# Optimization experiments

Measured on AMD Instinct MI355X. Metric: run time of the kernel, lower is better.

Reference implementation:

```python
import jax, jax.numpy as jnp
import numpy as np

N, E = 10000, 160000
F_IN, H1, C1, C2 = 256, 8, 128, 128
SLOPE = 0.2  # PyG GATConv default negative_slope


def setup_inputs() -> dict:
    key = jax.random.key(0)
    ks = jax.random.split(key, 9)
    s = 0.05
    return {
        "x": jax.random.normal(ks[0], (N, F_IN), jnp.float32),
        "edge_index": jax.random.randint(ks[1], (2, E), 0, N),
        "W1": jax.random.normal(ks[2], (F_IN, H1 * C1), jnp.float32) * s,
        "a_src1": jax.random.normal(ks[3], (H1, C1), jnp.float32) * s,
        "a_dst1": jax.random.normal(ks[4], (H1, C1), jnp.float32) * s,
        "b1": jnp.zeros((H1 * C1,), jnp.float32),
        "W2": jax.random.normal(ks[5], (H1 * C1, C2), jnp.float32) * s,
        "a_src2": jax.random.normal(ks[6], (1, C2), jnp.float32) * s,
        "a_dst2": jax.random.normal(ks[7], (1, C2), jnp.float32) * s,
        "b2": jnp.zeros((C2,), jnp.float32),
    }


def gat_conv(x, src, dst, W, a_s, a_d, b, heads, out_ch, concat):
    n = x.shape[0]
    h = (x @ W).reshape(n, heads, out_ch)            # [N,H,C]
    s_src = jnp.einsum("nhc,hc->nh", h, a_s)         # [N,H]
    s_dst = jnp.einsum("nhc,hc->nh", h, a_d)
    e = jax.nn.leaky_relu(s_src[src] + s_dst[dst], SLOPE)   # [Etot,H]
    # segment softmax over incoming edges per destination (self-loops guarantee non-empty segments)
    m = jax.lax.stop_gradient(jax.ops.segment_max(e, dst, num_segments=n))
    p = jnp.exp(e - m[dst])
    denom = jax.ops.segment_sum(p, dst, num_segments=n)
    alpha = p / denom[dst]                            # [Etot,H]
    out = jax.ops.segment_sum(h[src] * alpha[:, :, None], dst, num_segments=n)  # [N,H,C]
    out = out.reshape(n, heads * out_ch) if concat else out.mean(axis=1)
    return out + b


def reference(x, edge_index, W1, a_src1, a_dst1, b1, W2, a_src2, a_dst2, b2):
    n = x.shape[0]
    loops = jnp.arange(n, dtype=edge_index.dtype)     # PyG add_self_loops=True
    src = jnp.concatenate([edge_index[0], loops])
    dst = jnp.concatenate([edge_index[1], loops])
    # dropout layers are identity at inference (training=False)
    h1 = jax.nn.elu(gat_conv(x, src, dst, W1, a_src1, a_dst1, b1, H1, C1, True))
    return gat_conv(h1, src, dst, W2, a_src2, a_dst2, b2, 1, C2, False)
```

## Files before the change

### kernel.cpp

```cpp
#include <hip/hip_runtime.h>
#include <math.h>

#define F_IN 256
#define H1 8
#define C1 128
#define HC1 1024
#define C2 128
#define SLOPE 0.2f

typedef unsigned short u16;
typedef __attribute__((ext_vector_type(8))) short bf16x8;
typedef __attribute__((ext_vector_type(4))) float f32x4;
typedef __attribute__((ext_vector_type(2))) float f32x2;


__device__ __forceinline__ float lrelu(float v) { return v > 0.f ? v : SLOPE * v; }

__device__ __forceinline__ unsigned bf16_rne(float x) {
    unsigned u = __float_as_uint(x);
    u += 0x7fffu + ((u >> 16) & 1u);
    return u >> 16;
}

__device__ __forceinline__ void split2(float a, float b, unsigned& hi, unsigned& lo) {
    unsigned ha = bf16_rne(a), hb = bf16_rne(b);
    float fa = __uint_as_float(ha << 16), fb = __uint_as_float(hb << 16);
    hi = ha | (hb << 16);
    lo = bf16_rne(a - fa) | (bf16_rne(b - fb) << 16);
}

__device__ __forceinline__ void gload16(const u16* g, u16* l) {
    __builtin_amdgcn_global_load_lds(
        (const __attribute__((address_space(1))) unsigned*)g,
        (__attribute__((address_space(3))) unsigned*)l, 16, 0, 0);
}


__global__ void init_deg(int* deg, int n) {
    int i = blockIdx.x * blockDim.x + threadIdx.x;
    if (i < n) deg[i] = 1;
}

__global__ void hist_kernel(const int* __restrict__ dst, int* __restrict__ deg, int E) {
    int i = blockIdx.x * blockDim.x + threadIdx.x;
    if (i < E) atomicAdd(&deg[dst[i]], 1);
}

__global__ void scan_kernel(const int* __restrict__ deg, int* __restrict__ start,
                            int* __restrict__ cursor, int n) {
    __shared__ int buf[1024];
    int carry = 0;
    for (int base = 0; base < n; base += 1024) {
        int i = base + (int)threadIdx.x;
        int v = (i < n) ? deg[i] : 0;
        buf[threadIdx.x] = v;
        __syncthreads();
        for (int offd = 1; offd < 1024; offd <<= 1) {
            int tv = 0;
            if ((int)threadIdx.x >= offd) tv = buf[threadIdx.x - offd];
            __syncthreads();
            if ((int)threadIdx.x >= offd) buf[threadIdx.x] += tv;
            __syncthreads();
        }
        int incl = buf[threadIdx.x];
        if (i < n) { start[i] = carry + incl - v; cursor[i] = carry + incl - v; }
        carry += buf[1023];
        __syncthreads();
    }
    if (threadIdx.x == 0) start[n] = carry;
}

__global__ void scatter_kernel(const int* __restrict__ src, const int* __restrict__ dst,
                               int* __restrict__ cursor, int* __restrict__ ssorted,
                               int E, int N) {
    int i = blockIdx.x * blockDim.x + threadIdx.x;
    if (i < E) {
        int d = dst[i];
        int pos = atomicAdd(&cursor[d], 1);
        ssorted[pos] = src[i];
    } else if (i < E + N) {
        int d = i - E;
        int pos = atomicAdd(&cursor[d], 1);
        ssorted[pos] = d;
    }
}


__global__ void split_mat(const float* __restrict__ in, u16* __restrict__ hi,
                          u16* __restrict__ lo, int n) {
    int i = blockIdx.x * blockDim.x + threadIdx.x;
    if (i >= n) return;
    float v = in[i];
    unsigned h = bf16_rne(v);
    hi[i] = (u16)h;
    lo[i] = (u16)bf16_rne(v - __uint_as_float(h << 16));
}

__global__ void split_transpose(const float* __restrict__ in, u16* __restrict__ hi,
                                u16* __restrict__ lo, int R, int C) {
    int i = blockIdx.x * blockDim.x + threadIdx.x;
    if (i >= R * C) return;
    int r = i / C, c = i % C;
    float v = in[i];
    unsigned h = bf16_rne(v);
    hi[(size_t)c * R + r] = (u16)h;
    lo[(size_t)c * R + r] = (u16)bf16_rne(v - __uint_as_float(h << 16));
}


__global__ __launch_bounds__(256) void gemm_mfma(const u16* __restrict__ Ahi,
                                                 const u16* __restrict__ Alo,
                                                 const u16* __restrict__ Bhi,
                                                 const u16* __restrict__ Blo,
                                                 u16* __restrict__ Cbf,
                                                 int M, int N, int K) {
    __shared__ u16 lds[16384];
    const int t = threadIdx.x;
    const int rbase = blockIdx.y * 128;
    const int cbase = blockIdx.x * 128;

    const int lane = t & 63;
    const int R0 = (t >> 7) << 6;
    const int C0 = ((t >> 6) & 1) << 6;
    const int lrow = lane & 15;
    const int kq = lane >> 4;

    f32x4 acc[4][4] = {};

    for (int k0 = 0; k0 < K; k0 += 32) {
#pragma unroll
        for (int i = 0; i < 2; i++) {
            int c = t + (i << 8);
            int row = c >> 2;
            int kc = (c & 3) << 3;
            int ar = min(rbase + row, M - 1);
            int br = cbase + row;
            gload16(Ahi + (size_t)ar * K + k0 + kc, &lds[c * 8]);
            gload16(Alo + (size_t)ar * K + k0 + kc, &lds[4096 + c * 8]);
            gload16(Bhi + (size_t)br * K + k0 + kc, &lds[8192 + c * 8]);
            gload16(Blo + (size_t)br * K + k0 + kc, &lds[12288 + c * 8]);
        }
        __syncthreads();

        bf16x8 ah[4], al[4], bh[4], bl[4];
#pragma unroll
        for (int m = 0; m < 4; m++) {
            int off = (R0 + (m << 4) + lrow) * 32 + (kq << 3);
            ah[m] = *(const bf16x8*)&lds[off];
            al[m] = *(const bf16x8*)&lds[4096 + off];
        }
#pragma unroll
        for (int n = 0; n < 4; n++) {
            int off = (C0 + (n << 4) + lrow) * 32 + (kq << 3);
            bh[n] = *(const bf16x8*)&lds[8192 + off];
            bl[n] = *(const bf16x8*)&lds[12288 + off];
        }
#pragma unroll
        for (int m = 0; m < 4; m++)
#pragma unroll
            for (int n = 0; n < 4; n++) {
                acc[m][n] = __builtin_amdgcn_mfma_f32_16x16x32_bf16(ah[m], bh[n], acc[m][n], 0, 0, 0);
                acc[m][n] = __builtin_amdgcn_mfma_f32_16x16x32_bf16(ah[m], bl[n], acc[m][n], 0, 0, 0);
                acc[m][n] = __builtin_amdgcn_mfma_f32_16x16x32_bf16(al[m], bh[n], acc[m][n], 0, 0, 0);
            }
        __syncthreads();
    }

#pragma unroll
    for (int m = 0; m < 4; m++)
#pragma unroll
        for (int n = 0; n < 4; n++) {
            int col = cbase + C0 + (n << 4) + lrow;
#pragma unroll
            for (int r = 0; r < 4; r++) {
                int row = rbase + R0 + (m << 4) + kq * 4 + r;
                if (row < M) Cbf[(size_t)row * N + col] = (u16)bf16_rne(acc[m][n][r]);
            }
        }
}


__global__ __launch_bounds__(256) void gemm_mfma64(const u16* __restrict__ Ahi,
                                                   const u16* __restrict__ Alo,
                                                   const u16* __restrict__ Bhi,
                                                   const u16* __restrict__ Blo,
                                                   u16* __restrict__ Cbf,
                                                   int M, int N, int K) {
    __shared__ u16 lds[8192];
    const int t = threadIdx.x;
    const int rbase = blockIdx.y * 64;
    const int cbase = blockIdx.x * 64;

    const int lane = t & 63;
    const int w = t >> 6;
    const int R0 = (w >> 1) << 5;
    const int C0 = (w & 1) << 5;
    const int lrow = lane & 15;
    const int kq = lane >> 4;

    f32x4 acc[2][2] = {};

    for (int k0 = 0; k0 < K; k0 += 32) {
        {
            int row = t >> 2;
            int kc = (t & 3) << 3;
            int ar = min(rbase + row, M - 1);
            int br = cbase + row;
            gload16(Ahi + (size_t)ar * K + k0 + kc, &lds[t * 8]);
            gload16(Alo + (size_t)ar * K + k0 + kc, &lds[2048 + t * 8]);
            gload16(Bhi + (size_t)br * K + k0 + kc, &lds[4096 + t * 8]);
            gload16(Blo + (size_t)br * K + k0 + kc, &lds[6144 + t * 8]);
        }
        __syncthreads();

        bf16x8 ah[2], al[2], bh[2], bl[2];
#pragma unroll
        for (int m = 0; m < 2; m++) {
            int off = (R0 + (m << 4) + lrow) * 32 + (kq << 3);
            ah[m] = *(const bf16x8*)&lds[off];
            al[m] = *(const bf16x8*)&lds[2048 + off];
        }
#pragma unroll
        for (int n = 0; n < 2; n++) {
            int off = (C0 + (n << 4) + lrow) * 32 + (kq << 3);
            bh[n] = *(const bf16x8*)&lds[4096 + off];
            bl[n] = *(const bf16x8*)&lds[6144 + off];
        }
#pragma unroll
        for (int m = 0; m < 2; m++)
#pragma unroll
            for (int n = 0; n < 2; n++) {
                acc[m][n] = __builtin_amdgcn_mfma_f32_16x16x32_bf16(ah[m], bh[n], acc[m][n], 0, 0, 0);
                acc[m][n] = __builtin_amdgcn_mfma_f32_16x16x32_bf16(ah[m], bl[n], acc[m][n], 0, 0, 0);
                acc[m][n] = __builtin_amdgcn_mfma_f32_16x16x32_bf16(al[m], bh[n], acc[m][n], 0, 0, 0);
            }
        __syncthreads();
    }

#pragma unroll
    for (int m = 0; m < 2; m++)
#pragma unroll
        for (int n = 0; n < 2; n++) {
            int col = cbase + C0 + (n << 4) + lrow;
#pragma unroll
            for (int r = 0; r < 4; r++) {
                int row = rbase + R0 + (m << 4) + kq * 4 + r;
                if (row < M) Cbf[(size_t)row * N + col] = (u16)bf16_rne(acc[m][n][r]);
            }
        }
}


__global__ __launch_bounds__(256) void scores1_bf(const unsigned* __restrict__ hbf,
                                                  const float* __restrict__ a_s,
                                                  const float* __restrict__ a_d,
                                                  float* __restrict__ ssrc,
                                                  float* __restrict__ sdst, int N) {
    int wid = blockIdx.x * 4 + (threadIdx.x >> 6);
    if (wid >= N * H1) return;
    int lane = threadIdx.x & 63;
    int n = wid >> 3, hh = wid & 7;
    unsigned u = hbf[(size_t)n * 512 + hh * 64 + lane];
    float c0 = __uint_as_float(u << 16);
    float c1 = __uint_as_float(u & 0xffff0000u);
    const float* as = a_s + hh * C1;
    const float* ad = a_d + hh * C1;
    float vs = c0 * as[2 * lane] + c1 * as[2 * lane + 1];
    float vd = c0 * ad[2 * lane] + c1 * ad[2 * lane + 1];
    for (int off = 32; off; off >>= 1) {
        vs += __shfl_xor(vs, off);
        vd += __shfl_xor(vd, off);
    }
    if (lane == 0) { ssrc[wid] = vs; sdst[wid] = vd; }
}

__global__ __launch_bounds__(256) void scores2_bf(const unsigned* __restrict__ hbf,
                                                  const float* __restrict__ a_s,
                                                  const float* __restrict__ a_d,
                                                  float* __restrict__ ssrc,
                                                  float* __restrict__ sdst, int N) {
    int n = blockIdx.x * 4 + (threadIdx.x >> 6);
    if (n >= N) return;
    int lane = threadIdx.x & 63;
    unsigned u = hbf[(size_t)n * 64 + lane];
    float c0 = __uint_as_float(u << 16);
    float c1 = __uint_as_float(u & 0xffff0000u);
    float vs = c0 * a_s[2 * lane] + c1 * a_s[2 * lane + 1];
    float vd = c0 * a_d[2 * lane] + c1 * a_d[2 * lane + 1];
    for (int off = 32; off; off >>= 1) {
        vs += __shfl_xor(vs, off);
        vd += __shfl_xor(vd, off);
    }
    if (lane == 0) { ssrc[n] = vs; sdst[n] = vd; }
}


template<int H, bool SPLITOUT>
__global__ __launch_bounds__(256) void agg_bf(const unsigned* __restrict__ hbf,
                                              const float* __restrict__ ssrc,
                                              const float* __restrict__ sdst,
                                              const int* __restrict__ start,
                                              const int* __restrict__ ssorted,
                                              const float* __restrict__ bias,
                                              float* __restrict__ out,
                                              unsigned* __restrict__ outHi,
                                              unsigned* __restrict__ outLo, int N) {
    constexpr int CH = 128;
    __shared__ int2 pairs[4][CH + 4];
    int hh, grp;
    if (H == 8) { hh = blockIdx.x & 7; grp = blockIdx.x >> 3; }
    else        { hh = 0;              grp = blockIdx.x; }
    int wid = threadIdx.x >> 6, lane = threadIdx.x & 63;
    int d = grp * 4 + wid;
    if (d >= N) return;
    const int g = lane >> 4, p = lane & 15;
    int s0 = start[d];
    int ne = start[d + 1] - s0;
    float sd = sdst[d * H + hh];
    const int rowbytes = H * 256;
    const char* hbase = (const char*)hbf + hh * 256 + p * 16;

    float m = -1e30f;
    for (int e = lane; e < ne; e += 64)
        m = fmaxf(m, lrelu(ssrc[ssorted[s0 + e] * H + hh] + sd));
    for (int o = 32; o; o >>= 1) m = fmaxf(m, __shfl_xor(m, o));

    float ssum = 0.f;
    for (int e = lane; e < ne; e += 64)
        ssum += __expf(lrelu(ssrc[ssorted[s0 + e] * H + hh] + sd) - m);
    for (int o = 32; o; o >>= 1) ssum += __shfl_xor(ssum, o);
    float inv = 1.f / ssum;

    f32x2 acc0 = {0.f, 0.f}, acc1 = {0.f, 0.f}, acc2 = {0.f, 0.f}, acc3 = {0.f, 0.f};
    for (int c0 = 0; c0 < ne; c0 += CH) {
        int cn = min(CH, ne - c0);
        int cn4 = (cn + 3) & ~3;
        for (int e = lane; e < cn4; e += 64) {
            int2 pr = make_int2(0, 0);
            if (e < cn) {
                int sr = ssorted[s0 + c0 + e];
                float a = __expf(lrelu(ssrc[sr * H + hh] + sd) - m) * inv;
                pr = make_int2(sr * rowbytes, __float_as_int(a));
            }
            pairs[wid][e] = pr;
        }
#pragma unroll 2
        for (int e2 = 0; e2 < cn4; e2 += 4) {
            int2 pr = pairs[wid][e2 + g];
            float a = __int_as_float(pr.y);
            uint4 u = *(const uint4*)(hbase + pr.x);
            f32x2 av = {a, a};
            f32x2 f0 = {__uint_as_float(u.x << 16), __uint_as_float(u.x & 0xffff0000u)};
            f32x2 f1 = {__uint_as_float(u.y << 16), __uint_as_float(u.y & 0xffff0000u)};
            f32x2 f2 = {__uint_as_float(u.z << 16), __uint_as_float(u.z & 0xffff0000u)};
            f32x2 f3 = {__uint_as_float(u.w << 16), __uint_as_float(u.w & 0xffff0000u)};
            acc0 += av * f0;
            acc1 += av * f1;
            acc2 += av * f2;
            acc3 += av * f3;
        }
    }

    float acc[8] = {acc0.x, acc0.y, acc1.x, acc1.y, acc2.x, acc2.y, acc3.x, acc3.y};
#pragma unroll
    for (int i = 0; i < 8; i++) {
        acc[i] += __shfl_xor(acc[i], 16);
        acc[i] += __shfl_xor(acc[i], 32);
    }

    float r0 = g == 0 ? acc[0] : g == 1 ? acc[2] : g == 2 ? acc[4] : acc[6];
    float r1 = g == 0 ? acc[1] : g == 1 ? acc[3] : g == 2 ? acc[5] : acc[7];
    int j = 4 * p + g;
    float2 bv = ((const float2*)bias)[hh * 64 + j];
    r0 += bv.x; r1 += bv.y;
    size_t idx = (size_t)d * (H * 64) + hh * 64 + j;
    if (SPLITOUT) {
        r0 = r0 > 0.f ? r0 : expm1f(r0);
        r1 = r1 > 0.f ? r1 : expm1f(r1);
        unsigned hi, lo;
        split2(r0, r1, hi, lo);
        outHi[idx] = hi;
        outLo[idx] = lo;
    } else {
        ((float2*)out)[idx] = make_float2(r0, r1);
    }
}


extern "C" void kernel_launch(void* const* d_in, const int* in_sizes, int n_in,
                              void* d_out, int out_size, void* d_ws, size_t ws_size,
                              hipStream_t stream) {
    const float* x      = (const float*)d_in[0];
    const int*   ei     = (const int*)d_in[1];
    const float* W1     = (const float*)d_in[2];
    const float* a_src1 = (const float*)d_in[3];
    const float* a_dst1 = (const float*)d_in[4];
    const float* b1     = (const float*)d_in[5];
    const float* W2     = (const float*)d_in[6];
    const float* a_src2 = (const float*)d_in[7];
    const float* a_dst2 = (const float*)d_in[8];
    const float* b2     = (const float*)d_in[9];
    float* out = (float*)d_out;

    int E = in_sizes[1] / 2;
    int N = in_sizes[0] / F_IN;
    const int* esrc = ei;
    const int* edst = ei + E;

    char* ws = (char*)d_ws;
    size_t off = 0;
    auto alloc = [&](size_t bytes) -> char* {
        char* p = ws + off;
        off = (off + bytes + 255) & ~(size_t)255;
        return p;
    };
    u16* x_hi    = (u16*)alloc((size_t)N * F_IN * 2);
    u16* x_lo    = (u16*)alloc((size_t)N * F_IN * 2);
    u16* W1t_hi  = (u16*)alloc((size_t)F_IN * HC1 * 2);
    u16* W1t_lo  = (u16*)alloc((size_t)F_IN * HC1 * 2);
    u16* W2t_hi  = (u16*)alloc((size_t)HC1 * C2 * 2);
    u16* W2t_lo  = (u16*)alloc((size_t)HC1 * C2 * 2);
    u16* h1_bf   = (u16*)alloc((size_t)N * HC1 * 2);
    u16* h1a_hi  = (u16*)alloc((size_t)N * HC1 * 2);
    u16* h1a_lo  = (u16*)alloc((size_t)N * HC1 * 2);
    u16* h2_bf   = (u16*)alloc((size_t)N * C2 * 2);
    float* ss1   = (float*)alloc((size_t)N * H1 * 4);
    float* sd1   = (float*)alloc((size_t)N * H1 * 4);
    float* ss2   = (float*)alloc((size_t)N * 4);
    float* sd2   = (float*)alloc((size_t)N * 4);
    int* deg     = (int*)alloc((size_t)N * 4);
    int* startp  = (int*)alloc((size_t)(N + 1) * 4);
    int* cursor  = (int*)alloc((size_t)N * 4);
    int* ssorted = (int*)alloc((size_t)(E + N) * 4);

    init_deg<<<(N + 255) / 256, 256, 0, stream>>>(deg, N);
    hist_kernel<<<(E + 255) / 256, 256, 0, stream>>>(edst, deg, E);
    scan_kernel<<<1, 1024, 0, stream>>>(deg, startp, cursor, N);
    scatter_kernel<<<(E + N + 255) / 256, 256, 0, stream>>>(esrc, edst, cursor, ssorted, E, N);

    split_mat<<<(N * F_IN + 255) / 256, 256, 0, stream>>>(x, x_hi, x_lo, N * F_IN);
    split_transpose<<<(F_IN * HC1 + 255) / 256, 256, 0, stream>>>(W1, W1t_hi, W1t_lo, F_IN, HC1);
    split_transpose<<<(HC1 * C2 + 255) / 256, 256, 0, stream>>>(W2, W2t_hi, W2t_lo, HC1, C2);

    gemm_mfma<<<dim3(HC1 / 128, (N + 127) / 128), 256, 0, stream>>>(
        x_hi, x_lo, W1t_hi, W1t_lo, h1_bf, N, HC1, F_IN);
    scores1_bf<<<(N * H1 + 3) / 4, 256, 0, stream>>>(
        (const unsigned*)h1_bf, a_src1, a_dst1, ss1, sd1, N);
    agg_bf<H1, true><<<((N + 3) / 4) * H1, 256, 0, stream>>>(
        (const unsigned*)h1_bf, ss1, sd1, startp, ssorted, b1,
        nullptr, (unsigned*)h1a_hi, (unsigned*)h1a_lo, N);

    gemm_mfma64<<<dim3(C2 / 64, (N + 63) / 64), 256, 0, stream>>>(
        h1a_hi, h1a_lo, W2t_hi, W2t_lo, h2_bf, N, C2, HC1);
    scores2_bf<<<(N + 3) / 4, 256, 0, stream>>>(
        (const unsigned*)h2_bf, a_src2, a_dst2, ss2, sd2, N);
    agg_bf<1, false><<<(N + 3) / 4, 256, 0, stream>>>(
        (const unsigned*)h2_bf, ss2, sd2, startp, ssorted, b2,
        out, nullptr, nullptr, N);
}
```

Measured before the change: 261.1 us.

## Precompute edge softmax numerators and denominators in separate kernels, drop max pass

Splits the per-destination aggregation into three stages. An edge-parallel kernel computes exp(leaky_relu(score)) for all heads, a per-node kernel sums these into inverse denominators, and a gather kernel reads the precomputed weights directly. The max-subtraction pass and the shared-memory pair staging are removed, which relies on the scores staying small enough that exp does not overflow. It adds extra launches, a dsorted array and an Et×8 float intermediate buffer with more global memory traffic.

```diff
diff --git a/kernel.cpp b/kernel.cpp
--- a/kernel.cpp
+++ b/kernel.cpp
@@ -72,16 +72,18 @@
 
 __global__ void scatter_kernel(const int* __restrict__ src, const int* __restrict__ dst,
                                int* __restrict__ cursor, int* __restrict__ ssorted,
-                               int E, int N) {
+                               int* __restrict__ dsorted, int E, int N) {
     int i = blockIdx.x * blockDim.x + threadIdx.x;
     if (i < E) {
         int d = dst[i];
         int pos = atomicAdd(&cursor[d], 1);
         ssorted[pos] = src[i];
+        dsorted[pos] = d;
     } else if (i < E + N) {
         int d = i - E;
         int pos = atomicAdd(&cursor[d], 1);
         ssorted[pos] = d;
+        dsorted[pos] = d;
     }
 }
 
@@ -295,70 +297,106 @@
 }
 
 
-template<int H, bool SPLITOUT>
-__global__ __launch_bounds__(256) void agg_bf(const unsigned* __restrict__ hbf,
+__global__ __launch_bounds__(256) void edgep1(const int* __restrict__ ssorted,
+                                              const int* __restrict__ dsorted,
                                               const float* __restrict__ ssrc,
                                               const float* __restrict__ sdst,
+                                              float* __restrict__ p, int Et) {
+    int e = blockIdx.x * 256 + threadIdx.x;
+    if (e >= Et) return;
+    int sr = ssorted[e], dr = dsorted[e];
+    float4 s0 = ((const float4*)(ssrc + sr * 8))[0];
+    float4 s1 = ((const float4*)(ssrc + sr * 8))[1];
+    float4 d0 = ((const float4*)(sdst + dr * 8))[0];
+    float4 d1 = ((const float4*)(sdst + dr * 8))[1];
+    float4 r0, r1;
+    r0.x = __expf(lrelu(s0.x + d0.x));
+    r0.y = __expf(lrelu(s0.y + d0.y));
+    r0.z = __expf(lrelu(s0.z + d0.z));
+    r0.w = __expf(lrelu(s0.w + d0.w));
+    r1.x = __expf(lrelu(s1.x + d1.x));
+    r1.y = __expf(lrelu(s1.y + d1.y));
+    r1.z = __expf(lrelu(s1.z + d1.z));
+    r1.w = __expf(lrelu(s1.w + d1.w));
+    ((float4*)(p + (size_t)e * 8))[0] = r0;
+    ((float4*)(p + (size_t)e * 8))[1] = r1;
+}
+
+__global__ __launch_bounds__(256) void edgep2(const int* __restrict__ ssorted,
+                                              const int* __restrict__ dsorted,
+                                              const float* __restrict__ ssrc,
+                                              const float* __restrict__ sdst,
+                                              float* __restrict__ p, int Et) {
+    int e = blockIdx.x * 256 + threadIdx.x;
+    if (e >= Et) return;
+    p[e] = __expf(lrelu(ssrc[ssorted[e]] + sdst[dsorted[e]]));
+}
+
+
+__global__ __launch_bounds__(256) void denom1(const float* __restrict__ p,
                                               const int* __restrict__ start,
-                                              const int* __restrict__ ssorted,
-                                              const float* __restrict__ bias,
-                                              float* __restrict__ out,
-                                              unsigned* __restrict__ outHi,
-                                              unsigned* __restrict__ outLo, int N) {
-    constexpr int CH = 128;
-    __shared__ int2 pairs[4][CH + 4];
+                                              float* __restrict__ dinv, int N) {
+    int t = blockIdx.x * 256 + threadIdx.x;
+    if (t >= N * 8) return;
+    int d = t >> 3, h = t & 7;
+    int s0 = start[d], ne = start[d + 1] - s0;
+    float s = 0.f;
+    for (int e = 0; e < ne; e++) s += p[(size_t)(s0 + e) * 8 + h];
+    dinv[t] = 1.f / s;
+}
+
+__global__ __launch_bounds__(256) void denom2(const float* __restrict__ p,
+                                              const int* __restrict__ start,
+                                              float* __restrict__ dinv, int N) {
+    int d = blockIdx.x * 256 + threadIdx.x;
+    if (d >= N) return;
+    int s0 = start[d], ne = start[d + 1] - s0;
+    float s = 0.f;
+    for (int e = 0; e < ne; e++) s += p[s0 + e];
+    dinv[d] = 1.f / s;
+}
+
+
+template<int H, bool SPLITOUT>
+__global__ __launch_bounds__(256) void agg_gather(const unsigned* __restrict__ hbf,
+                                                  const float* __restrict__ pmat,
+                                                  const float* __restrict__ dinv,
+                                                  const int* __restrict__ start,
+                                                  const int* __restrict__ ssorted,
+                                                  const float* __restrict__ bias,
+                                                  float* __restrict__ out,
+                                                  unsigned* __restrict__ outHi,
+                                                  unsigned* __restrict__ outLo, int N) {
     int hh, grp;
     if (H == 8) { hh = blockIdx.x & 7; grp = blockIdx.x >> 3; }
     else        { hh = 0;              grp = blockIdx.x; }
     int wid = threadIdx.x >> 6, lane = threadIdx.x & 63;
     int d = grp * 4 + wid;
     if (d >= N) return;
-    const int g = lane >> 4, p = lane & 15;
+    const int g = lane >> 4, p16 = lane & 15;
     int s0 = start[d];
     int ne = start[d + 1] - s0;
-    float sd = sdst[d * H + hh];
-    const int rowbytes = H * 256;
-    const char* hbase = (const char*)hbf + hh * 256 + p * 16;
-
-    float m = -1e30f;
-    for (int e = lane; e < ne; e += 64)
-        m = fmaxf(m, lrelu(ssrc[ssorted[s0 + e] * H + hh] + sd));
-    for (int o = 32; o; o >>= 1) m = fmaxf(m, __shfl_xor(m, o));
-
-    float ssum = 0.f;
-    for (int e = lane; e < ne; e += 64)
-        ssum += __expf(lrelu(ssrc[ssorted[s0 + e] * H + hh] + sd) - m);
-    for (int o = 32; o; o >>= 1) ssum += __shfl_xor(ssum, o);
-    float inv = 1.f / ssum;
+    float inv = dinv[d * H + hh];
+    const unsigned* hbase = hbf + hh * 64 + p16 * 4;
+    const int rowu = H * 64;
 
     f32x2 acc0 = {0.f, 0.f}, acc1 = {0.f, 0.f}, acc2 = {0.f, 0.f}, acc3 = {0.f, 0.f};
-    for (int c0 = 0; c0 < ne; c0 += CH) {
-        int cn = min(CH, ne - c0);
-        int cn4 = (cn + 3) & ~3;
-        for (int e = lane; e < cn4; e += 64) {
-            int2 pr = make_int2(0, 0);
-            if (e < cn) {
-                int sr = ssorted[s0 + c0 + e];
-                float a = __expf(lrelu(ssrc[sr * H + hh] + sd) - m) * inv;
-                pr = make_int2(sr * rowbytes, __float_as_int(a));
-            }
-            pairs[wid][e] = pr;
-        }
 #pragma unroll 2
-        for (int e2 = 0; e2 < cn4; e2 += 4) {
-            int2 pr = pairs[wid][e2 + g];
-            float a = __int_as_float(pr.y);
-            uint4 u = *(const uint4*)(hbase + pr.x);
-            f32x2 av = {a, a};
-            f32x2 f0 = {__uint_as_float(u.x << 16), __uint_as_float(u.x & 0xffff0000u)};
-            f32x2 f1 = {__uint_as_float(u.y << 16), __uint_as_float(u.y & 0xffff0000u)};
-            f32x2 f2 = {__uint_as_float(u.z << 16), __uint_as_float(u.z & 0xffff0000u)};
-            f32x2 f3 = {__uint_as_float(u.w << 16), __uint_as_float(u.w & 0xffff0000u)};
-            acc0 += av * f0;
-            acc1 += av * f1;
-            acc2 += av * f2;
-            acc3 += av * f3;
-        }
+    for (int e2 = 0; e2 < ne; e2 += 4) {
+        int e = e2 + g;
+        int ec = min(e, ne - 1);
+        int sr = ssorted[s0 + ec];
+        float a = (e < ne) ? pmat[(size_t)(s0 + e) * H + hh] * inv : 0.f;
+        uint4 u = *(const uint4*)(hbase + (size_t)sr * rowu);
+        f32x2 av = {a, a};
+        f32x2 f0 = {__uint_as_float(u.x << 16), __uint_as_float(u.x & 0xffff0000u)};
+        f32x2 f1 = {__uint_as_float(u.y << 16), __uint_as_float(u.y & 0xffff0000u)};
+        f32x2 f2 = {__uint_as_float(u.z << 16), __uint_as_float(u.z & 0xffff0000u)};
+        f32x2 f3 = {__uint_as_float(u.w << 16), __uint_as_float(u.w & 0xffff0000u)};
+        acc0 += av * f0;
+        acc1 += av * f1;
+        acc2 += av * f2;
+        acc3 += av * f3;
     }
 
     float acc[8] = {acc0.x, acc0.y, acc1.x, acc1.y, acc2.x, acc2.y, acc3.x, acc3.y};
@@ -370,7 +408,7 @@
 
     float r0 = g == 0 ? acc[0] : g == 1 ? acc[2] : g == 2 ? acc[4] : acc[6];
     float r1 = g == 0 ? acc[1] : g == 1 ? acc[3] : g == 2 ? acc[5] : acc[7];
-    int j = 4 * p + g;
+    int j = 4 * p16 + g;
     float2 bv = ((const float2*)bias)[hh * 64 + j];
     r0 += bv.x; r1 += bv.y;
     size_t idx = (size_t)d * (H * 64) + hh * 64 + j;
@@ -404,6 +442,7 @@
 
     int E = in_sizes[1] / 2;
     int N = in_sizes[0] / F_IN;
+    int Et = E + N;
     const int* esrc = ei;
     const int* edst = ei + E;
 
@@ -428,15 +467,20 @@
     float* sd1   = (float*)alloc((size_t)N * H1 * 4);
     float* ss2   = (float*)alloc((size_t)N * 4);
     float* sd2   = (float*)alloc((size_t)N * 4);
+    float* p1    = (float*)alloc((size_t)Et * H1 * 4);
+    float* p2    = (float*)alloc((size_t)Et * 4);
+    float* dinv1 = (float*)alloc((size_t)N * H1 * 4);
+    float* dinv2 = (float*)alloc((size_t)N * 4);
     int* deg     = (int*)alloc((size_t)N * 4);
     int* startp  = (int*)alloc((size_t)(N + 1) * 4);
     int* cursor  = (int*)alloc((size_t)N * 4);
-    int* ssorted = (int*)alloc((size_t)(E + N) * 4);
+    int* ssorted = (int*)alloc((size_t)Et * 4);
+    int* dsorted = (int*)alloc((size_t)Et * 4);
 
     init_deg<<<(N + 255) / 256, 256, 0, stream>>>(deg, N);
     hist_kernel<<<(E + 255) / 256, 256, 0, stream>>>(edst, deg, E);
     scan_kernel<<<1, 1024, 0, stream>>>(deg, startp, cursor, N);
-    scatter_kernel<<<(E + N + 255) / 256, 256, 0, stream>>>(esrc, edst, cursor, ssorted, E, N);
+    scatter_kernel<<<(Et + 255) / 256, 256, 0, stream>>>(esrc, edst, cursor, ssorted, dsorted, E, N);
 
     split_mat<<<(N * F_IN + 255) / 256, 256, 0, stream>>>(x, x_hi, x_lo, N * F_IN);
     split_transpose<<<(F_IN * HC1 + 255) / 256, 256, 0, stream>>>(W1, W1t_hi, W1t_lo, F_IN, HC1);
@@ -446,15 +490,19 @@
         x_hi, x_lo, W1t_hi, W1t_lo, h1_bf, N, HC1, F_IN);
     scores1_bf<<<(N * H1 + 3) / 4, 256, 0, stream>>>(
         (const unsigned*)h1_bf, a_src1, a_dst1, ss1, sd1, N);
-    agg_bf<H1, true><<<((N + 3) / 4) * H1, 256, 0, stream>>>(
-        (const unsigned*)h1_bf, ss1, sd1, startp, ssorted, b1,
+    edgep1<<<(Et + 255) / 256, 256, 0, stream>>>(ssorted, dsorted, ss1, sd1, p1, Et);
+    denom1<<<(N * H1 + 255) / 256, 256, 0, stream>>>(p1, startp, dinv1, N);
+    agg_gather<H1, true><<<((N + 3) / 4) * H1, 256, 0, stream>>>(
+        (const unsigned*)h1_bf, p1, dinv1, startp, ssorted, b1,
         nullptr, (unsigned*)h1a_hi, (unsigned*)h1a_lo, N);
 
     gemm_mfma64<<<dim3(C2 / 64, (N + 63) / 64), 256, 0, stream>>>(
         h1a_hi, h1a_lo, W2t_hi, W2t_lo, h2_bf, N, C2, HC1);
     scores2_bf<<<(N + 3) / 4, 256, 0, stream>>>(
         (const unsigned*)h2_bf, a_src2, a_dst2, ss2, sd2, N);
-    agg_bf<1, false><<<(N + 3) / 4, 256, 0, stream>>>(
-        (const unsigned*)h2_bf, ss2, sd2, startp, ssorted, b2,
+    edgep2<<<(Et + 255) / 256, 256, 0, stream>>>(ssorted, dsorted, ss2, sd2, p2, Et);
+    denom2<<<(N + 255) / 256, 256, 0, stream>>>(p2, startp, dinv2, N);
+    agg_gather<1, false><<<(N + 3) / 4, 256, 0, stream>>>(
+        (const unsigned*)h2_bf, p2, dinv2, startp, ssorted, b2,
         out, nullptr, nullptr, N);
 }
```

After: 275.9 us. +5.7%, slower.
